# Optimization experiments

Hardware: AMD Instinct MI355X
Metric: run time of the kernel (lower is better)

The kernel has to match this reference:

```python
import jax, jax.numpy as jnp
import numpy as np


def setup_inputs() -> dict:
    key = jax.random.key(0)
    ks = jax.random.split(key, 13)
    B, T, F = 4096, 512, 64
    P, M = 64, 64  # price / metrics embedding dims
    TD, ED = 1, 8  # target_dim, explanatory_dim
    s = 0.05
    return {
        "input_seq": jax.random.normal(ks[0], (B, T, F), jnp.float32),
        "m_Wih": jax.random.normal(ks[1], (M, F + P), jnp.float32) * s,
        "m_Whh": jax.random.normal(ks[2], (M, M), jnp.float32) * s,
        "m_bih": jax.random.normal(ks[3], (M,), jnp.float32) * s,
        "m_bhh": jax.random.normal(ks[4], (M,), jnp.float32) * s,
        "p_Wih": jax.random.normal(ks[5], (P, F + M), jnp.float32) * s,
        "p_Whh": jax.random.normal(ks[6], (P, P), jnp.float32) * s,
        "p_bih": jax.random.normal(ks[7], (P,), jnp.float32) * s,
        "p_bhh": jax.random.normal(ks[8], (P,), jnp.float32) * s,
        "price_lin_W": jax.random.normal(ks[9], (TD, P), jnp.float32) * s,
        "price_lin_b": jax.random.normal(ks[10], (TD,), jnp.float32) * s,
        "metrics_lin_W": jax.random.normal(ks[11], (ED, M), jnp.float32) * s,
        "metrics_lin_b": jax.random.normal(ks[12], (ED,), jnp.float32) * s,
    }


def reference(input_seq, m_Wih, m_Whh, m_bih, m_bhh,
              p_Wih, p_Whh, p_bih, p_bhh,
              price_lin_W, price_lin_b, metrics_lin_W, metrics_lin_b):
    B = input_seq.shape[0]
    P = p_Whh.shape[0]
    M = m_Whh.shape[0]
    p0 = jnp.zeros((B, P), input_seq.dtype)
    m0 = jnp.zeros((B, M), input_seq.dtype)

    def step(carry, x_t):  # x_t: [B, F]
        p, m = carry
        # metrics cell: input = cat(x_t, price_embedding)
        m = jnp.tanh(jnp.concatenate([x_t, p], axis=1) @ m_Wih.T + m_bih
                     + m @ m_Whh.T + m_bhh)
        # price cell: input = cat(x_t, metrics_embedding)
        p = jnp.tanh(jnp.concatenate([x_t, m], axis=1) @ p_Wih.T + p_bih
                     + p @ p_Whh.T + p_bhh)
        return (p, m), None

    (p, m), _ = jax.lax.scan(step, (p0, m0), jnp.swapaxes(input_seq, 0, 1))
    # dropout in eval mode = identity
    price_pred = p @ price_lin_W.T + price_lin_b
    metrics_pred = m @ metrics_lin_W.T + metrics_lin_b
    return (price_pred, metrics_pred)
```

## Files before the change

### kernel.cpp

```cpp
#include <hip/hip_runtime.h>

typedef short bf16x8 __attribute__((ext_vector_type(8)));
typedef float f32x4 __attribute__((ext_vector_type(4)));
typedef int   int4v  __attribute__((ext_vector_type(4)));

#define MFMA16(a, b, c) __builtin_amdgcn_mfma_f32_16x16x32_bf16((a), (b), (c), 0, 0, 0)

static constexpr int T_LEN = 512;
static constexpr int F_DIM = 64;
static constexpr int NB    = 16;
static constexpr float C1  = 2.885390081777927f;

__device__ __forceinline__ unsigned short brne(float f) {
  unsigned u = __float_as_uint(f);
  return (unsigned short)((u + 0x7fffu + ((u >> 16) & 1u)) >> 16);
}

__device__ __forceinline__ unsigned short rhu(float f) {
  return (unsigned short)((__float_as_uint(f) + 0x8000u) >> 16);
}

__device__ __forceinline__ int cvtpk(float lo, float hi) {
  int r;
  asm("v_cvt_pk_bf16_f32 %0, %1, %2" : "=v"(r) : "v"(lo), "v"(hi));
  return r;
}

__device__ __forceinline__ bf16x8 cvt8(const float4 &a, const float4 &b) {
  int4v d = {cvtpk(a.x, a.y), cvtpk(a.z, a.w), cvtpk(b.x, b.y), cvtpk(b.z, b.w)};
  union { int4v i; bf16x8 h; } u;
  u.i = d;
  return u.h;
}

__device__ __forceinline__ float tanh_fold(float s, float c2) {
  float e  = __builtin_amdgcn_exp2f(__builtin_fmaf(s, C1, c2));
  float rc = __builtin_amdgcn_rcpf(e + 1.0f);
  return __builtin_fmaf(-2.0f, rc, 1.0f);
}

__device__ __forceinline__ void bar() {
  asm volatile("s_waitcnt lgkmcnt(0)" ::: "memory");
  __builtin_amdgcn_s_barrier();
  __builtin_amdgcn_sched_barrier(0);
}

template<bool FIN>
__device__ __forceinline__ void step_cells(
    int arow, int g8, int j, int rowb,
    const bf16x8 &x0, const bf16x8 &x1,
    bf16x8 &mo0, bf16x8 &mo1,
    const bf16x8 (&Bm)[6], const bf16x8 (&Bp)[6],
    float c2m, float c2p, const f32x4 &Z,
    unsigned short (*sm)[72],
    unsigned short (*sp_c)[72], unsigned short (*sp_p)[72],
    float (*mfin)[68], float (*pfin)[68])
{
  bf16x8 p0 = *(const bf16x8 *)&sp_p[arow][g8];
  bf16x8 p1 = *(const bf16x8 *)&sp_p[arow][32 + g8];

  f32x4 a0 = MFMA16(x0, Bm[0], Z);
  f32x4 a1 = MFMA16(x1, Bm[1], Z);
  a0 = MFMA16(mo0, Bm[4], a0);
  a1 = MFMA16(mo1, Bm[5], a1);
  a0 = MFMA16(p0, Bm[2], a0);
  a1 = MFMA16(p1, Bm[3], a1);
  f32x4 b0 = MFMA16(x0, Bp[0], Z);
  f32x4 b1 = MFMA16(x1, Bp[1], Z);
  b0 = MFMA16(p0, Bp[4], b0);
  b1 = MFMA16(p1, Bp[5], b1);
#pragma unroll
  for (int r = 0; r < 4; ++r) {
    float tv = tanh_fold(a0[r] + a1[r], c2m);
    sm[rowb + r][j] = rhu(tv);
    if (FIN) mfin[rowb + r][j] = tv;
  }
  bar();
  {
    bf16x8 n0 = *(const bf16x8 *)&sm[arow][g8];
    bf16x8 n1 = *(const bf16x8 *)&sm[arow][32 + g8];
    b0 = MFMA16(n0, Bp[2], b0);
    b1 = MFMA16(n1, Bp[3], b1);
    mo0 = n0;
    mo1 = n1;
#pragma unroll
    for (int r = 0; r < 4; ++r) {
      float tv = tanh_fold(b0[r] + b1[r], c2p);
      sp_c[rowb + r][j] = rhu(tv);
      if (FIN) pfin[rowb + r][j] = tv;
    }
  }
  bar();
}

__global__ __launch_bounds__(256, 1)
void mr_rnn_kernel(const float *__restrict__ x,
                   const float *__restrict__ mWih, const float *__restrict__ mWhh,
                   const float *__restrict__ mbih, const float *__restrict__ mbhh,
                   const float *__restrict__ pWih, const float *__restrict__ pWhh,
                   const float *__restrict__ pbih, const float *__restrict__ pbhh,
                   const float *__restrict__ plW,  const float *__restrict__ plb,
                   const float *__restrict__ mlW,  const float *__restrict__ mlb,
                   float *__restrict__ out, int B)
{
  __shared__ __align__(16) unsigned short sm[NB][72];
  __shared__ __align__(16) unsigned short sp[2][NB][72];
  __shared__ __align__(16) float s_mfin[NB][68], s_pfin[NB][68];

  const int tid  = threadIdx.x;
  const int lane = tid & 63;
  const int q    = tid >> 6;
  const int l15  = lane & 15;
  const int arow = l15;
  const int g    = lane >> 4;
  const int j    = q * 16 + l15;
  const int b0   = blockIdx.x * NB;
  const int g8   = g * 8;
  const int rowb = g * 4;

  bf16x8 Bm[6], Bp[6];
#pragma unroll
  for (int kt = 0; kt < 6; ++kt) {
    const int k0 = kt * 32 + g8;
#pragma unroll
    for (int i = 0; i < 8; ++i) {
      const int k = k0 + i;
      float wm = (k < 128) ? mWih[j * 128 + k] : mWhh[j * 64 + (k - 128)];
      float wp = (k < 128) ? pWih[j * 128 + k] : pWhh[j * 64 + (k - 128)];
      Bm[kt][i] = (short)brne(wm);
      Bp[kt][i] = (short)brne(wp);
    }
  }
  const float c2m = C1 * (mbih[j] + mbhh[j]);
  const float c2p = C1 * (pbih[j] + pbhh[j]);
  const f32x4 Z = {0.f, 0.f, 0.f, 0.f};

  for (int idx = tid; idx < NB * 72; idx += 256) {
    const int bb = idx / 72, kk = idx % 72;
    sp[1][bb][kk] = 0;
  }
  bf16x8 mo0 = {0, 0, 0, 0, 0, 0, 0, 0};
  bf16x8 mo1 = {0, 0, 0, 0, 0, 0, 0, 0};

  const float *pxl = x + (size_t)(b0 + arow) * T_LEN * F_DIM + g8;
  float4 Q0 = *(const float4 *)(pxl);
  float4 Q1 = *(const float4 *)(pxl + 4);
  float4 Q2 = *(const float4 *)(pxl + 32);
  float4 Q3 = *(const float4 *)(pxl + 36);
  bf16x8 x0 = cvt8(Q0, Q1);
  bf16x8 x1 = cvt8(Q2, Q3);
  float4 R0 = *(const float4 *)(pxl + F_DIM);
  float4 R1 = *(const float4 *)(pxl + F_DIM + 4);
  float4 R2 = *(const float4 *)(pxl + F_DIM + 32);
  float4 R3 = *(const float4 *)(pxl + F_DIM + 36);
  __syncthreads();

#pragma unroll 1
  for (int t = 0; t < T_LEN - 2; t += 2) {
    Q0 = *(const float4 *)(pxl + 2 * F_DIM);
    Q1 = *(const float4 *)(pxl + 2 * F_DIM + 4);
    Q2 = *(const float4 *)(pxl + 2 * F_DIM + 32);
    Q3 = *(const float4 *)(pxl + 2 * F_DIM + 36);
    step_cells<false>(arow, g8, j, rowb, x0, x1, mo0, mo1,
                      Bm, Bp, c2m, c2p, Z,
                      sm, sp[0], sp[1], s_mfin, s_pfin);
    x0 = cvt8(R0, R1);
    x1 = cvt8(R2, R3);
    R0 = *(const float4 *)(pxl + 3 * F_DIM);
    R1 = *(const float4 *)(pxl + 3 * F_DIM + 4);
    R2 = *(const float4 *)(pxl + 3 * F_DIM + 32);
    R3 = *(const float4 *)(pxl + 3 * F_DIM + 36);
    step_cells<false>(arow, g8, j, rowb, x0, x1, mo0, mo1,
                      Bm, Bp, c2m, c2p, Z,
                      sm, sp[1], sp[0], s_mfin, s_pfin);
    x0 = cvt8(Q0, Q1);
    x1 = cvt8(Q2, Q3);
    pxl += 2 * F_DIM;
  }
  step_cells<false>(arow, g8, j, rowb, x0, x1, mo0, mo1,
                    Bm, Bp, c2m, c2p, Z,
                    sm, sp[0], sp[1], s_mfin, s_pfin);
  x0 = cvt8(R0, R1);
  x1 = cvt8(R2, R3);
  step_cells<true>(arow, g8, j, rowb, x0, x1, mo0, mo1,
                   Bm, Bp, c2m, c2p, Z,
                   sm, sp[1], sp[0], s_mfin, s_pfin);
  __syncthreads();

  if (tid < NB) {
    const int b = tid;
    float acc = plb[0];
#pragma unroll 1
    for (int k = 0; k < 64; ++k) acc += s_pfin[b][k] * plW[k];
    out[b0 + b] = acc;
  } else if (tid < NB + NB * 8) {
    const int r = tid - NB;
    const int b = r >> 3, e = r & 7;
    float acc = mlb[e];
#pragma unroll 1
    for (int k = 0; k < 64; ++k) acc += s_mfin[b][k] * mlW[e * 64 + k];
    out[(size_t)B + (size_t)(b0 + b) * 8 + e] = acc;
  }
}

extern "C" void kernel_launch(void* const* d_in, const int* in_sizes, int n_in,
                              void* d_out, int out_size, void* d_ws, size_t ws_size,
                              hipStream_t stream) {
  (void)n_in; (void)out_size; (void)d_ws; (void)ws_size;
  const float* x    = (const float*)d_in[0];
  const float* mWih = (const float*)d_in[1];
  const float* mWhh = (const float*)d_in[2];
  const float* mbih = (const float*)d_in[3];
  const float* mbhh = (const float*)d_in[4];
  const float* pWih = (const float*)d_in[5];
  const float* pWhh = (const float*)d_in[6];
  const float* pbih = (const float*)d_in[7];
  const float* pbhh = (const float*)d_in[8];
  const float* plW  = (const float*)d_in[9];
  const float* plb  = (const float*)d_in[10];
  const float* mlW  = (const float*)d_in[11];
  const float* mlb  = (const float*)d_in[12];
  const int B = in_sizes[0] / (T_LEN * F_DIM);
  const int nblk = B / NB;
  mr_rnn_kernel<<<dim3(nblk), dim3(256), 0, stream>>>(
      x, mWih, mWhh, mbih, mbhh, pWih, pWhh, pbih, pbhh,
      plW, plb, mlW, mlb, (float*)d_out, B);
}
```

Before: 268.3 us.

## Switch to single-wave blocks of four batch rows, dropping block barriers

Restructures the recurrence so each 64-thread block (one wavefront) handles 4 batch rows and computes all 64 output columns itself. The MFMA A-operand rows are replicated across the 16-row tile (row = lane&3) and each lane selects its own column result. This removes the two s_barrier calls per time step, replacing cross-wave sync with intra-wave LDS exchange. The cost is four times the MFMA work per useful output, many more weight registers per lane (48 bf16x8 vectors), and 1024 blocks that rely on high occupancy to hide latency.

Result: slower. 589.8 us (+119.8%).

```diff
diff --git a/kernel.cpp b/kernel.cpp
--- a/kernel.cpp
+++ b/kernel.cpp
@@ -8,7 +8,7 @@
 
 static constexpr int T_LEN = 512;
 static constexpr int F_DIM = 64;
-static constexpr int NB    = 16;
+static constexpr int RPB   = 4;
 static constexpr float C1  = 2.885390081777927f;
 
 __device__ __forceinline__ unsigned short brne(float f) {
@@ -39,61 +39,54 @@
   return __builtin_fmaf(-2.0f, rc, 1.0f);
 }
 
-__device__ __forceinline__ void bar() {
-  asm volatile("s_waitcnt lgkmcnt(0)" ::: "memory");
-  __builtin_amdgcn_s_barrier();
-  __builtin_amdgcn_sched_barrier(0);
-}
-
 template<bool FIN>
-__device__ __forceinline__ void step_cells(
-    int arow, int g8, int j, int rowb,
+__device__ __forceinline__ void cell(
     const bf16x8 &x0, const bf16x8 &x1,
-    bf16x8 &mo0, bf16x8 &mo1,
-    const bf16x8 (&Bm)[6], const bf16x8 (&Bp)[6],
-    float c2m, float c2p, const f32x4 &Z,
-    unsigned short (*sm)[72],
-    unsigned short (*sp_c)[72], unsigned short (*sp_p)[72],
-    float (*mfin)[68], float (*pfin)[68])
+    const bf16x8 &o0, const bf16x8 &o1,
+    bf16x8 &d0, bf16x8 &d1,
+    const bf16x8 (&W)[4][6],
+    unsigned short (*rbuf)[72], unsigned short (*wbuf)[72],
+    float (*fin)[64], float c2,
+    int br, int g8, int G, int lane, const f32x4 &Z)
 {
-  bf16x8 p0 = *(const bf16x8 *)&sp_p[arow][g8];
-  bf16x8 p1 = *(const bf16x8 *)&sp_p[arow][32 + g8];
-
-  f32x4 a0 = MFMA16(x0, Bm[0], Z);
-  f32x4 a1 = MFMA16(x1, Bm[1], Z);
-  a0 = MFMA16(mo0, Bm[4], a0);
-  a1 = MFMA16(mo1, Bm[5], a1);
-  a0 = MFMA16(p0, Bm[2], a0);
-  a1 = MFMA16(p1, Bm[3], a1);
-  f32x4 b0 = MFMA16(x0, Bp[0], Z);
-  f32x4 b1 = MFMA16(x1, Bp[1], Z);
-  b0 = MFMA16(p0, Bp[4], b0);
-  b1 = MFMA16(p1, Bp[5], b1);
-#pragma unroll
-  for (int r = 0; r < 4; ++r) {
-    float tv = tanh_fold(a0[r] + a1[r], c2m);
-    sm[rowb + r][j] = rhu(tv);
-    if (FIN) mfin[rowb + r][j] = tv;
-  }
-  bar();
-  {
-    bf16x8 n0 = *(const bf16x8 *)&sm[arow][g8];
-    bf16x8 n1 = *(const bf16x8 *)&sm[arow][32 + g8];
-    b0 = MFMA16(n0, Bp[2], b0);
-    b1 = MFMA16(n1, Bp[3], b1);
-    mo0 = n0;
-    mo1 = n1;
-#pragma unroll
-    for (int r = 0; r < 4; ++r) {
-      float tv = tanh_fold(b0[r] + b1[r], c2p);
-      sp_c[rowb + r][j] = rhu(tv);
-      if (FIN) pfin[rowb + r][j] = tv;
-    }
-  }
-  bar();
-}
-
-__global__ __launch_bounds__(256, 1)
+  d0 = *(const bf16x8 *)&rbuf[br][g8];
+  d1 = *(const bf16x8 *)&rbuf[br][32 + g8];
+  f32x4 a0 = MFMA16(x0, W[0][0], Z);
+  f32x4 a1 = MFMA16(x0, W[1][0], Z);
+  f32x4 a2 = MFMA16(x0, W[2][0], Z);
+  f32x4 a3 = MFMA16(x0, W[3][0], Z);
+  a0 = MFMA16(x1, W[0][1], a0);
+  a1 = MFMA16(x1, W[1][1], a1);
+  a2 = MFMA16(x1, W[2][1], a2);
+  a3 = MFMA16(x1, W[3][1], a3);
+  a0 = MFMA16(o0, W[0][4], a0);
+  a1 = MFMA16(o0, W[1][4], a1);
+  a2 = MFMA16(o0, W[2][4], a2);
+  a3 = MFMA16(o0, W[3][4], a3);
+  a0 = MFMA16(o1, W[0][5], a0);
+  a1 = MFMA16(o1, W[1][5], a1);
+  a2 = MFMA16(o1, W[2][5], a2);
+  a3 = MFMA16(o1, W[3][5], a3);
+  a0 = MFMA16(d0, W[0][2], a0);
+  a1 = MFMA16(d0, W[1][2], a1);
+  a2 = MFMA16(d0, W[2][2], a2);
+  a3 = MFMA16(d0, W[3][2], a3);
+  a0 = MFMA16(d1, W[0][3], a0);
+  a1 = MFMA16(d1, W[1][3], a1);
+  a2 = MFMA16(d1, W[2][3], a2);
+  a3 = MFMA16(d1, W[3][3], a3);
+#pragma unroll
+  for (int q = 0; q < 4; ++q) {
+    float s01 = (G & 1) ? a1[q] : a0[q];
+    float s23 = (G & 1) ? a3[q] : a2[q];
+    float z   = (G & 2) ? s23 : s01;
+    float tv  = tanh_fold(z, c2);
+    wbuf[q][lane] = rhu(tv);
+    if (FIN) fin[q][lane] = tv;
+  }
+}
+
+__global__ __launch_bounds__(64, 1)
 void mr_rnn_kernel(const float *__restrict__ x,
                    const float *__restrict__ mWih, const float *__restrict__ mWhh,
                    const float *__restrict__ mbih, const float *__restrict__ mbhh,
@@ -103,46 +96,44 @@
                    const float *__restrict__ mlW,  const float *__restrict__ mlb,
                    float *__restrict__ out, int B)
 {
-  __shared__ __align__(16) unsigned short sm[NB][72];
-  __shared__ __align__(16) unsigned short sp[2][NB][72];
-  __shared__ __align__(16) float s_mfin[NB][68], s_pfin[NB][68];
-
-  const int tid  = threadIdx.x;
-  const int lane = tid & 63;
-  const int q    = tid >> 6;
+  __shared__ __align__(16) unsigned short mT[RPB][72], pT[RPB][72];
+  __shared__ __align__(16) float s_mfin[RPB][64], s_pfin[RPB][64];
+
+  const int lane = threadIdx.x;
   const int l15  = lane & 15;
-  const int arow = l15;
-  const int g    = lane >> 4;
-  const int j    = q * 16 + l15;
-  const int b0   = blockIdx.x * NB;
-  const int g8   = g * 8;
-  const int rowb = g * 4;
-
-  bf16x8 Bm[6], Bp[6];
-#pragma unroll
-  for (int kt = 0; kt < 6; ++kt) {
-    const int k0 = kt * 32 + g8;
-#pragma unroll
-    for (int i = 0; i < 8; ++i) {
-      const int k = k0 + i;
-      float wm = (k < 128) ? mWih[j * 128 + k] : mWhh[j * 64 + (k - 128)];
-      float wp = (k < 128) ? pWih[j * 128 + k] : pWhh[j * 64 + (k - 128)];
-      Bm[kt][i] = (short)brne(wm);
-      Bp[kt][i] = (short)brne(wp);
+  const int br   = lane & 3;
+  const int G    = lane >> 4;
+  const int g8   = G * 8;
+  const int b0   = blockIdx.x * RPB;
+
+  bf16x8 Bm[4][6], Bp[4][6];
+#pragma unroll
+  for (int ct = 0; ct < 4; ++ct) {
+    const int j = ct * 16 + l15;
+#pragma unroll
+    for (int kt = 0; kt < 6; ++kt) {
+      const int k0 = kt * 32 + g8;
+#pragma unroll
+      for (int i = 0; i < 8; ++i) {
+        const int k = k0 + i;
+        float wm = (k < 128) ? mWih[j * 128 + k] : mWhh[j * 64 + (k - 128)];
+        float wp = (k < 128) ? pWih[j * 128 + k] : pWhh[j * 64 + (k - 128)];
+        Bm[ct][kt][i] = (short)brne(wm);
+        Bp[ct][kt][i] = (short)brne(wp);
+      }
     }
   }
-  const float c2m = C1 * (mbih[j] + mbhh[j]);
-  const float c2p = C1 * (pbih[j] + pbhh[j]);
+  const float c2m = C1 * (mbih[lane] + mbhh[lane]);
+  const float c2p = C1 * (pbih[lane] + pbhh[lane]);
   const f32x4 Z = {0.f, 0.f, 0.f, 0.f};
 
-  for (int idx = tid; idx < NB * 72; idx += 256) {
-    const int bb = idx / 72, kk = idx % 72;
-    sp[1][bb][kk] = 0;
-  }
+#pragma unroll
+  for (int q = 0; q < RPB; ++q) pT[q][lane] = 0;
   bf16x8 mo0 = {0, 0, 0, 0, 0, 0, 0, 0};
   bf16x8 mo1 = {0, 0, 0, 0, 0, 0, 0, 0};
-
-  const float *pxl = x + (size_t)(b0 + arow) * T_LEN * F_DIM + g8;
+  bf16x8 po0, po1;
+
+  const float *pxl = x + (size_t)(b0 + br) * T_LEN * F_DIM + g8;
   float4 Q0 = *(const float4 *)(pxl);
   float4 Q1 = *(const float4 *)(pxl + 4);
   float4 Q2 = *(const float4 *)(pxl + 32);
@@ -153,7 +144,6 @@
   float4 R1 = *(const float4 *)(pxl + F_DIM + 4);
   float4 R2 = *(const float4 *)(pxl + F_DIM + 32);
   float4 R3 = *(const float4 *)(pxl + F_DIM + 36);
-  __syncthreads();
 
 #pragma unroll 1
   for (int t = 0; t < T_LEN - 2; t += 2) {
@@ -161,40 +151,43 @@
     Q1 = *(const float4 *)(pxl + 2 * F_DIM + 4);
     Q2 = *(const float4 *)(pxl + 2 * F_DIM + 32);
     Q3 = *(const float4 *)(pxl + 2 * F_DIM + 36);
-    step_cells<false>(arow, g8, j, rowb, x0, x1, mo0, mo1,
-                      Bm, Bp, c2m, c2p, Z,
-                      sm, sp[0], sp[1], s_mfin, s_pfin);
+    cell<false>(x0, x1, mo0, mo1, po0, po1, Bm, pT, mT, s_mfin, c2m,
+                br, g8, G, lane, Z);
+    cell<false>(x0, x1, po0, po1, mo0, mo1, Bp, mT, pT, s_pfin, c2p,
+                br, g8, G, lane, Z);
     x0 = cvt8(R0, R1);
     x1 = cvt8(R2, R3);
     R0 = *(const float4 *)(pxl + 3 * F_DIM);
     R1 = *(const float4 *)(pxl + 3 * F_DIM + 4);
     R2 = *(const float4 *)(pxl + 3 * F_DIM + 32);
     R3 = *(const float4 *)(pxl + 3 * F_DIM + 36);
-    step_cells<false>(arow, g8, j, rowb, x0, x1, mo0, mo1,
-                      Bm, Bp, c2m, c2p, Z,
-                      sm, sp[1], sp[0], s_mfin, s_pfin);
+    cell<false>(x0, x1, mo0, mo1, po0, po1, Bm, pT, mT, s_mfin, c2m,
+                br, g8, G, lane, Z);
+    cell<false>(x0, x1, po0, po1, mo0, mo1, Bp, mT, pT, s_pfin, c2p,
+                br, g8, G, lane, Z);
     x0 = cvt8(Q0, Q1);
     x1 = cvt8(Q2, Q3);
     pxl += 2 * F_DIM;
   }
-  step_cells<false>(arow, g8, j, rowb, x0, x1, mo0, mo1,
-                    Bm, Bp, c2m, c2p, Z,
-                    sm, sp[0], sp[1], s_mfin, s_pfin);
+  cell<false>(x0, x1, mo0, mo1, po0, po1, Bm, pT, mT, s_mfin, c2m,
+              br, g8, G, lane, Z);
+  cell<false>(x0, x1, po0, po1, mo0, mo1, Bp, mT, pT, s_pfin, c2p,
+              br, g8, G, lane, Z);
   x0 = cvt8(R0, R1);
   x1 = cvt8(R2, R3);
-  step_cells<true>(arow, g8, j, rowb, x0, x1, mo0, mo1,
-                   Bm, Bp, c2m, c2p, Z,
-                   sm, sp[1], sp[0], s_mfin, s_pfin);
-  __syncthreads();
-
-  if (tid < NB) {
-    const int b = tid;
+  cell<true>(x0, x1, mo0, mo1, po0, po1, Bm, pT, mT, s_mfin, c2m,
+             br, g8, G, lane, Z);
+  cell<true>(x0, x1, po0, po1, mo0, mo1, Bp, mT, pT, s_pfin, c2p,
+             br, g8, G, lane, Z);
+
+  if (lane < RPB) {
+    const int b = lane;
     float acc = plb[0];
 #pragma unroll 1
     for (int k = 0; k < 64; ++k) acc += s_pfin[b][k] * plW[k];
     out[b0 + b] = acc;
-  } else if (tid < NB + NB * 8) {
-    const int r = tid - NB;
+  } else if (lane < RPB + RPB * 8) {
+    const int r = lane - RPB;
     const int b = r >> 3, e = r & 7;
     float acc = mlb[e];
 #pragma unroll 1
@@ -221,8 +214,8 @@
   const float* mlW  = (const float*)d_in[11];
   const float* mlb  = (const float*)d_in[12];
   const int B = in_sizes[0] / (T_LEN * F_DIM);
-  const int nblk = B / NB;
-  mr_rnn_kernel<<<dim3(nblk), dim3(256), 0, stream>>>(
+  const int nblk = B / RPB;
+  mr_rnn_kernel<<<dim3(nblk), dim3(64), 0, stream>>>(
       x, mWih, mWhh, mbih, mbhh, pWih, pWhh, pbih, pbhh,
       plW, plb, mlW, mlb, (float*)d_out, B);
 }
```
